# Kernel optimization log

Hardware: AMD Instinct MI355X
Metric: run time of the kernel (lower is better)

Reference implementation:

```python
import jax, jax.numpy as jnp
import numpy as np

N = 50000      # num nodes
E = 800000     # num edges
F_IN = 100     # input features (ogbn-products)
HID = 128      # hidden_dim (per-head out_channels)
H = 2          # heads
OUT = 47       # num classes
NEG_SLOPE = 0.2


def setup_inputs() -> dict:
    key = jax.random.key(0)
    ks = jax.random.split(key, 14)
    def glorot(k, shape, fan):
        return jax.random.normal(k, shape, jnp.float32) * (1.0 / np.sqrt(fan))
    x = jax.random.normal(ks[0], (N, F_IN), jnp.float32)
    edge_index = jax.random.randint(ks[1], (2, E), 0, N)
    # GAT layer 0: lin_l (= lin_r, shared) weight [H*HID, F_IN], attention vecs [H, HID]
    W0 = glorot(ks[2], (H * HID, F_IN), F_IN)
    b0 = jnp.zeros((H * HID,), jnp.float32)
    attl0 = glorot(ks[3], (H, HID), HID)
    attr0 = glorot(ks[4], (H, HID), HID)
    # GAT layer 1: input dim H*HID
    W1 = glorot(ks[5], (H * HID, H * HID), H * HID)
    b1 = jnp.zeros((H * HID,), jnp.float32)
    attl1 = glorot(ks[6], (H, HID), HID)
    attr1 = glorot(ks[7], (H, HID), HID)
    # post_mp: Linear(H*HID -> HID), Linear(HID -> OUT)
    Wp1 = glorot(ks[8], (HID, H * HID), H * HID)
    bp1 = jnp.zeros((HID,), jnp.float32)
    Wp2 = glorot(ks[9], (OUT, HID), HID)
    bp2 = jnp.zeros((OUT,), jnp.float32)
    return dict(x=x, edge_index=edge_index, W0=W0, b0=b0, attl0=attl0, attr0=attr0,
                W1=W1, b1=b1, attl1=attl1, attr1=attr1,
                Wp1=Wp1, bp1=bp1, Wp2=Wp2, bp2=bp2)


def gat_layer(x, W, b, att_l, att_r, src, dst):
    # shared lin_l == lin_r in the source
    h = (x @ W.T + b).reshape(-1, H, HID)          # [N, H, C]
    alpha_l = jnp.einsum('nhc,hc->nh', h, att_l)   # per-node left scores
    alpha_r = jnp.einsum('nhc,hc->nh', h, att_r)   # per-node right scores
    e = jax.nn.leaky_relu(alpha_l[src] + alpha_r[dst], NEG_SLOPE)  # [E, H]
    # segment softmax over edges grouped by destination node
    emax = jax.ops.segment_max(e, dst, num_segments=N)             # [N, H]
    ee = jnp.exp(e - emax[dst])
    denom = jax.ops.segment_sum(ee, dst, num_segments=N)           # [N, H]
    a = ee / denom[dst]                                            # [E, H]
    msg = a[:, :, None] * h[src]                                   # [E, H, C]
    out = jax.ops.segment_sum(msg, dst, num_segments=N)            # [N, H, C]
    return out.reshape(-1, H * HID)


def reference(x, edge_index, W0, b0, attl0, attr0, W1, b1, attl1, attr1, Wp1, bp1, Wp2, bp2):
    src, dst = edge_index[0], edge_index[1]
    x = jax.nn.relu(gat_layer(x, W0, b0, attl0, attr0, src, dst))
    x = jax.nn.relu(gat_layer(x, W1, b1, attl1, attr1, src, dst))
    h = x @ Wp1.T + bp1           # dropout p=0.0 -> identity
    logits = h @ Wp2.T + bp2
    return jax.nn.log_softmax(logits, axis=1)
```

## Files before the change

### kernel.cpp

```cpp
#include <hip/hip_runtime.h>
#include <math.h>

#define N_NODES 50000
#define E_EDGES 800000
#define F_IN 100
#define HID 128
#define HEADS 2
#define OUT_C 47
#define HH (HEADS*HID)
#define MPAD 50048

typedef float floatx4 __attribute__((ext_vector_type(4)));
typedef float float2v __attribute__((ext_vector_type(2)));
typedef short short8 __attribute__((ext_vector_type(8)));

__device__ inline ushort bf16round(float v) {
    unsigned u = __float_as_uint(v);
    return (ushort)((u + 0x7FFFu + ((u >> 16) & 1u)) >> 16);
}

__device__ __forceinline__ void gl_lds16(const void* g, void* l) {
    __builtin_amdgcn_global_load_lds(
        (const __attribute__((address_space(1))) unsigned int*)g,
        (__attribute__((address_space(3))) unsigned int*)l, 16, 0, 0);
}

__device__ __forceinline__ void gemm_body(
    int bx, int by,
    const ushort* __restrict__ Ab, const ushort* __restrict__ Wb,
    const float* __restrict__ bias,
    ushort* __restrict__ Hb,
    const float* __restrict__ attl, const float* __restrict__ attr,
    float* __restrict__ al, float* __restrict__ ar,
    int M, int Kp, ushort* sA, ushort* sB)
{
    const int t = threadIdx.x;
    const int wave = t >> 6, lane = t & 63;
    const int quad = lane >> 4, l16 = lane & 15;
    const int rl = lane >> 2, seg = lane & 3;
    const int m0 = by * 128, n0 = bx * 128;

    floatx4 acc[2][8];
#pragma unroll
    for (int i = 0; i < 2; i++)
#pragma unroll
        for (int j = 0; j < 8; j++) acc[i][j] = (floatx4)(0.f);

    for (int k0 = 0; k0 < Kp; k0 += 32) {
#pragma unroll
        for (int j = 0; j < 2; j++) {
            int br = wave * 32 + j * 16;
            size_t gro = (size_t)(m0 + br + rl) * Kp + k0 + seg * 8;
            gl_lds16(Ab + gro, sA + br * 32);
        }
#pragma unroll
        for (int j = 0; j < 2; j++) {
            int br = wave * 32 + j * 16;
            size_t gro = (size_t)(n0 + br + rl) * Kp + k0 + seg * 8;
            gl_lds16(Wb + gro, sB + br * 32);
        }
        __syncthreads();

        short8 af[2];
#pragma unroll
        for (int sm = 0; sm < 2; sm++) {
            int r = wave * 32 + sm * 16 + l16;
            af[sm] = *(const short8*)(sA + r * 32 + quad * 8);
        }
#pragma unroll
        for (int sn = 0; sn < 8; sn++) {
            int r = sn * 16 + l16;
            short8 b = *(const short8*)(sB + r * 32 + quad * 8);
#pragma unroll
            for (int sm = 0; sm < 2; sm++)
                acc[sm][sn] = __builtin_amdgcn_mfma_f32_16x16x32_bf16(af[sm], b, acc[sm][sn], 0, 0, 0);
        }
        __syncthreads();
    }

    float bias_r[8], att_l[8], att_r[8];
#pragma unroll
    for (int sn = 0; sn < 8; sn++) {
        int ai = n0 + sn * 16 + l16;
        bias_r[sn] = bias[ai];
        att_l[sn] = attl[ai];
        att_r[sn] = attr[ai];
    }
#pragma unroll
    for (int sm = 0; sm < 2; sm++)
#pragma unroll
        for (int r = 0; r < 4; r++) {
            int gm = m0 + wave * 32 + sm * 16 + quad * 4 + r;
            float suml = 0.f, sumr = 0.f;
#pragma unroll
            for (int sn = 0; sn < 8; sn++) {
                float v = acc[sm][sn][r] + bias_r[sn];
                suml += v * att_l[sn];
                sumr += v * att_r[sn];
                if (gm < M) {
                    int gn = n0 + sn * 16 + l16;
                    Hb[(size_t)gm * 256 + gn] = bf16round(v);
                }
            }
#pragma unroll
            for (int off = 1; off < 16; off <<= 1) {
                suml += __shfl_xor(suml, off);
                sumr += __shfl_xor(sumr, off);
            }
            if (l16 == 0 && gm < M) {
                al[gm * HEADS + bx] = suml;
                ar[gm * HEADS + bx] = sumr;
            }
        }
}

__global__ __launch_bounds__(256) void gemm_l0(
    const ushort* __restrict__ xb, const ushort* __restrict__ W0b,
    const float* __restrict__ b0,
    const float* __restrict__ attl0, const float* __restrict__ attr0,
    ushort* __restrict__ hb, float* __restrict__ al, float* __restrict__ ar)
{
    __shared__ ushort sA[128 * 32], sB[128 * 32];
    gemm_body(blockIdx.x, blockIdx.y, xb, W0b, b0,
              hb, attl0, attr0, al, ar, N_NODES, 128, sA, sB);
}

__global__ __launch_bounds__(256) void gemm_l1(
    const ushort* __restrict__ Ab, const ushort* __restrict__ Wb,
    const float* __restrict__ bias, ushort* __restrict__ Hb,
    const float* __restrict__ attl, const float* __restrict__ attr,
    float* __restrict__ al, float* __restrict__ ar)
{
    __shared__ ushort sA[128 * 32], sB[128 * 32];
    gemm_body(blockIdx.x, blockIdx.y, Ab, Wb, bias,
              Hb, attl, attr, al, ar, N_NODES, HH, sA, sB);
}

__global__ void count_convert(const int* __restrict__ dstv, int* __restrict__ deg,
                              ushort* __restrict__ rank,
                              const float* __restrict__ x,  const float* __restrict__ W0,
                              const float* __restrict__ W1, const float* __restrict__ Wp1,
                              const float* __restrict__ Wp2,
                              ushort* __restrict__ xb,  ushort* __restrict__ W0b,
                              ushort* __restrict__ W1b, ushort* __restrict__ Wp1b,
                              ushort* __restrict__ Wp2b) {
    const int cx = N_NODES * 32;
    const int c0 = cx + 256 * 32;
    const int c1 = c0 + (HH * HH) / 4;
    const int c2 = c1 + (HID * HH) / 4;
    const int c3 = c2 + (64 * HID) / 4;
    int i = blockIdx.x * 256 + threadIdx.x;
    if (i < E_EDGES) {
        int d = dstv[i];
        rank[i] = (ushort)atomicAdd(&deg[d], 1);
    }
    if (i >= c3) return;
    float4 v = make_float4(0.f, 0.f, 0.f, 0.f);
    ushort* H; size_t o;
    if (i < cx) {
        int row = i >> 5, kc = (i & 31) * 4;
        if (kc < F_IN) v = *(const float4*)(x + (size_t)row * F_IN + kc);
        H = xb; o = (size_t)row * 128 + kc;
    } else if (i < c0) {
        int j = i - cx;
        int row = j >> 5, kc = (j & 31) * 4;
        if (kc < F_IN) v = *(const float4*)(W0 + (size_t)row * F_IN + kc);
        H = W0b; o = (size_t)row * 128 + kc;
    } else if (i < c1) {
        int j = i - c0;
        v = *(const float4*)(W1 + (size_t)j * 4);
        H = W1b; o = (size_t)j * 4;
    } else if (i < c2) {
        int j = i - c1;
        v = *(const float4*)(Wp1 + (size_t)j * 4);
        H = Wp1b; o = (size_t)j * 4;
    } else {
        int j = i - c2;
        int row = j >> 5;
        if (row < OUT_C) v = *(const float4*)(Wp2 + (size_t)j * 4);
        H = Wp2b; o = (size_t)j * 4;
    }
    ushort4 r;
    r.x = bf16round(v.x); r.y = bf16round(v.y);
    r.z = bf16round(v.z); r.w = bf16round(v.w);
    *(ushort4*)(H + o) = r;
}

__global__ void scan_local(const int* __restrict__ cnt, int* __restrict__ excl,
                           int* __restrict__ bsum, int Nn) {
    __shared__ int s[256];
    int t = threadIdx.x;
    int i = blockIdx.x * 256 + t;
    int v = (i < Nn) ? cnt[i] : 0;
    s[t] = v;
    __syncthreads();
    for (int off = 1; off < 256; off <<= 1) {
        int add = (t >= off) ? s[t - off] : 0;
        __syncthreads();
        s[t] += add;
        __syncthreads();
    }
    int incl = s[t];
    if (i < Nn) excl[i] = incl - v;
    if (t == 255) bsum[blockIdx.x] = incl;
}

__global__ void scan_add_fused(int* __restrict__ rowptr, const int* __restrict__ bsum,
                               int Nn, int Etot, int nblk) {
    __shared__ int s[256];
    int t = threadIdx.x;
    s[t] = (t < nblk) ? bsum[t] : 0;
    __syncthreads();
    for (int off = 1; off < 256; off <<= 1) {
        int add = (t >= off) ? s[t - off] : 0;
        __syncthreads();
        s[t] += add;
        __syncthreads();
    }
    int add = (blockIdx.x == 0) ? 0 : s[blockIdx.x - 1];
    int i = blockIdx.x * 256 + t;
    if (i < Nn) rowptr[i] += add;
    if (i == 0) rowptr[Nn] = Etot;
}

__global__ void fill_csr16(const int* __restrict__ src, const int* __restrict__ dst,
                           const int* __restrict__ rowptr, const ushort* __restrict__ rank,
                           ushort* __restrict__ csr16, int E) {
    int e = blockIdx.x * 256 + threadIdx.x;
    if (e < E) {
        int pos = rowptr[dst[e]] + (int)rank[e];
        csr16[pos] = (ushort)src[e];
    }
}

__global__ __launch_bounds__(256) void gat_aggregate(
    const ushort* __restrict__ hb, const float* __restrict__ al, const float* __restrict__ ar,
    const int* __restrict__ rowptr, const ushort* __restrict__ csr16,
    ushort* __restrict__ outb)
{
    const int node = blockIdx.x * 4 + (threadIdx.x >> 6);
    const int lane = threadIdx.x & 63;
    if (node >= N_NODES) return;
    const int beg = rowptr[node], end = rowptr[node + 1];
    const int half = lane >> 5;
    const int l32  = lane & 31;
    const int headf = l32 >> 4;
    const float2 ard = ((const float2*)ar)[node];

    float dsum0 = 0.f, dsum1 = 0.f;
    float2v av[4];
#pragma unroll
    for (int j = 0; j < 4; j++) av[j] = (float2v)(0.f);

    for (int c0 = beg; c0 < end; c0 += 64) {
        const int n = min(64, end - c0);
        int s = 0; float w0 = 0.f, w1 = 0.f;
        if (lane < n) {
            s = (int)csr16[c0 + lane];
            float2 aa = ((const float2*)al)[s];
            float e0 = aa.x + ard.x;
            float e1 = aa.y + ard.y;
            e0 = fmaxf(e0, 0.f) + 0.2f * fminf(e0, 0.f);
            e1 = fmaxf(e1, 0.f) + 0.2f * fminf(e1, 0.f);
            w0 = __expf(e0); w1 = __expf(e1);
            dsum0 += w0; dsum1 += w1;
        }
        for (int i = 0; i < n; i += 4) {
            int e0i = i + half;
            int   se0 = __shfl(s,  e0i);
            float u00 = __shfl(w0, e0i);
            float u01 = __shfl(w1, e0i);
            float2v we0 = (float2v)(headf ? u01 : u00);
            const uint4 q0 = *(const uint4*)(hb + (size_t)se0 * 256 + l32 * 8);
            int e1i = i + 2 + half;
            int   se1 = __shfl(s,  e1i);
            float u10 = __shfl(w0, e1i);
            float u11 = __shfl(w1, e1i);
            float2v we1 = (float2v)(headf ? u11 : u10);
            const uint4 q1 = *(const uint4*)(hb + (size_t)se1 * 256 + l32 * 8);
            float2v p;
            p.x = __uint_as_float(q0.x << 16); p.y = __uint_as_float(q0.x & 0xFFFF0000u);
            av[0] += we0 * p;
            p.x = __uint_as_float(q0.y << 16); p.y = __uint_as_float(q0.y & 0xFFFF0000u);
            av[1] += we0 * p;
            p.x = __uint_as_float(q0.z << 16); p.y = __uint_as_float(q0.z & 0xFFFF0000u);
            av[2] += we0 * p;
            p.x = __uint_as_float(q0.w << 16); p.y = __uint_as_float(q0.w & 0xFFFF0000u);
            av[3] += we0 * p;
            p.x = __uint_as_float(q1.x << 16); p.y = __uint_as_float(q1.x & 0xFFFF0000u);
            av[0] += we1 * p;
            p.x = __uint_as_float(q1.y << 16); p.y = __uint_as_float(q1.y & 0xFFFF0000u);
            av[1] += we1 * p;
            p.x = __uint_as_float(q1.z << 16); p.y = __uint_as_float(q1.z & 0xFFFF0000u);
            av[2] += we1 * p;
            p.x = __uint_as_float(q1.w << 16); p.y = __uint_as_float(q1.w & 0xFFFF0000u);
            av[3] += we1 * p;
        }
    }
#pragma unroll
    for (int j = 0; j < 4; j++) {
        av[j].x += __shfl_xor(av[j].x, 32);
        av[j].y += __shfl_xor(av[j].y, 32);
    }
#pragma unroll
    for (int off = 32; off; off >>= 1) {
        dsum0 += __shfl_xor(dsum0, off);
        dsum1 += __shfl_xor(dsum1, off);
    }
    if (half == 0) {
        const float den = headf ? dsum1 : dsum0;
        const float inv = (end > beg) ? 1.f / den : 0.f;
        ushort r[8];
#pragma unroll
        for (int j = 0; j < 4; j++) {
            r[2*j]   = bf16round(fmaxf(av[j].x * inv, 0.f));
            r[2*j+1] = bf16round(fmaxf(av[j].y * inv, 0.f));
        }
        *(uint4*)(outb + (size_t)node * 256 + l32 * 8) = *(uint4*)r;
    }
}

__global__ __launch_bounds__(256) void fused_post(
    const ushort* __restrict__ Ab,
    const ushort* __restrict__ Bb,
    const float* __restrict__ bp1,
    const ushort* __restrict__ W2b,
    const float* __restrict__ bp2,
    float* __restrict__ out, int M)
{
    __shared__ ushort sA[128 * 32];
    __shared__ ushort sB[128 * 32];
    __shared__ ushort sP[128 * 136];

    const int t = threadIdx.x;
    const int wave = t >> 6, lane = t & 63;
    const int quad = lane >> 4, l16 = lane & 15;
    const int rl = lane >> 2, seg = lane & 3;
    const int m0 = blockIdx.x * 128;

    floatx4 acc[2][8];
#pragma unroll
    for (int i = 0; i < 2; i++)
#pragma unroll
        for (int j = 0; j < 8; j++) acc[i][j] = (floatx4)(0.f);

    for (int k0 = 0; k0 < HH; k0 += 32) {
#pragma unroll
        for (int j = 0; j < 2; j++) {
            int br = wave * 32 + j * 16;
            size_t gro = (size_t)(m0 + br + rl) * HH + k0 + seg * 8;
            gl_lds16(Ab + gro, sA + br * 32);
        }
#pragma unroll
        for (int j = 0; j < 2; j++) {
            int br = wave * 32 + j * 16;
            size_t gro = (size_t)(br + rl) * HH + k0 + seg * 8;
            gl_lds16(Bb + gro, sB + br * 32);
        }
        __syncthreads();
        short8 af[2];
#pragma unroll
        for (int sm = 0; sm < 2; sm++) {
            int r = wave * 32 + sm * 16 + l16;
            af[sm] = *(const short8*)(sA + r * 32 + quad * 8);
        }
#pragma unroll
        for (int sn = 0; sn < 8; sn++) {
            int r = sn * 16 + l16;
            short8 b = *(const short8*)(sB + r * 32 + quad * 8);
#pragma unroll
            for (int sm = 0; sm < 2; sm++)
                acc[sm][sn] = __builtin_amdgcn_mfma_f32_16x16x32_bf16(af[sm], b, acc[sm][sn], 0, 0, 0);
        }
        __syncthreads();
    }
#pragma unroll
    for (int sm = 0; sm < 2; sm++)
#pragma unroll
        for (int sn = 0; sn < 8; sn++)
#pragma unroll
            for (int r = 0; r < 4; r++) {
                int row = wave * 32 + sm * 16 + quad * 4 + r;
                int col = sn * 16 + l16;
                sP[row * 136 + col] = bf16round(acc[sm][sn][r] + bp1[col]);
            }
    __syncthreads();

    floatx4 acc2[2][4];
#pragma unroll
    for (int i = 0; i < 2; i++)
#pragma unroll
        for (int j = 0; j < 4; j++) acc2[i][j] = (floatx4)(0.f);

    for (int k0 = 0; k0 < HID; k0 += 32) {
        {
            int br = wave * 16;
            size_t gro = (size_t)(br + rl) * HID + k0 + seg * 8;
            gl_lds16(W2b + gro, sA + br * 32);
        }
        __syncthreads();
        short8 ph[2];
#pragma unroll
        for (int sm = 0; sm < 2; sm++) {
            int r = wave * 32 + sm * 16 + l16;
            ph[sm] = *(const short8*)(sP + r * 136 + k0 + quad * 8);
        }
#pragma unroll
        for (int sn = 0; sn < 4; sn++) {
            int r = sn * 16 + l16;
            short8 b = *(const short8*)(sA + r * 32 + quad * 8);
#pragma unroll
            for (int sm = 0; sm < 2; sm++)
                acc2[sm][sn] = __builtin_amdgcn_mfma_f32_16x16x32_bf16(ph[sm], b, acc2[sm][sn], 0, 0, 0);
        }
        __syncthreads();
    }

    float b2[4];
#pragma unroll
    for (int sn = 0; sn < 4; sn++) {
        int n = sn * 16 + l16;
        b2[sn] = (n < OUT_C) ? bp2[n] : 0.f;
    }
#pragma unroll
    for (int sm = 0; sm < 2; sm++)
#pragma unroll
        for (int r = 0; r < 4; r++) {
            float v[4];
            float m = -INFINITY;
#pragma unroll
            for (int sn = 0; sn < 4; sn++) {
                int n = sn * 16 + l16;
                float xv = (n < OUT_C) ? acc2[sm][sn][r] + b2[sn] : -INFINITY;
                v[sn] = xv;
                m = fmaxf(m, xv);
            }
#pragma unroll
            for (int off = 1; off < 16; off <<= 1) m = fmaxf(m, __shfl_xor(m, off));
            float ssum = 0.f;
#pragma unroll
            for (int sn = 0; sn < 4; sn++) {
                int n = sn * 16 + l16;
                if (n < OUT_C) ssum += __expf(v[sn] - m);
            }
#pragma unroll
            for (int off = 1; off < 16; off <<= 1) ssum += __shfl_xor(ssum, off);
            float lse = m + logf(ssum);
            int gm = m0 + wave * 32 + sm * 16 + quad * 4 + r;
            if (gm < M) {
#pragma unroll
                for (int sn = 0; sn < 4; sn++) {
                    int n = sn * 16 + l16;
                    if (n < OUT_C) out[(size_t)gm * OUT_C + n] = v[sn] - lse;
                }
            }
        }
}

extern "C" void kernel_launch(void* const* d_in, const int* in_sizes, int n_in,
                              void* d_out, int out_size, void* d_ws, size_t ws_size,
                              hipStream_t stream) {
    const float* x     = (const float*)d_in[0];
    const int*   ei    = (const int*)d_in[1];
    const float* W0    = (const float*)d_in[2];
    const float* b0    = (const float*)d_in[3];
    const float* attl0 = (const float*)d_in[4];
    const float* attr0 = (const float*)d_in[5];
    const float* W1    = (const float*)d_in[6];
    const float* b1    = (const float*)d_in[7];
    const float* attl1 = (const float*)d_in[8];
    const float* attr1 = (const float*)d_in[9];
    const float* Wp1   = (const float*)d_in[10];
    const float* bp1   = (const float*)d_in[11];
    const float* Wp2   = (const float*)d_in[12];
    const float* bp2   = (const float*)d_in[13];
    float* out = (float*)d_out;

    const int Nn = N_NODES, Etot = E_EDGES;
    const int* srcv = ei;
    const int* dstv = ei + Etot;

    char* ws = (char*)d_ws;
    size_t off = 0;
    auto alloc = [&](size_t bytes) -> void* {
        void* p = ws + off;
        off = (off + bytes + 255) & ~(size_t)255;
        return p;
    };
    int*    rowptr = (int*)alloc((size_t)(Nn + 1) * sizeof(int));
    int*    deg    = (int*)alloc((size_t)Nn * sizeof(int));
    ushort* rank   = (ushort*)alloc((size_t)Etot * 2);
    ushort* csr16  = (ushort*)alloc((size_t)Etot * 2);
    int*    bsum   = (int*)alloc(256 * sizeof(int));
    float*  al     = (float*)alloc((size_t)Nn * HEADS * sizeof(float));
    float*  ar     = (float*)alloc((size_t)Nn * HEADS * sizeof(float));
    ushort* xb     = (ushort*)alloc((size_t)MPAD * 128 * 2);
    ushort* W0b    = (ushort*)alloc((size_t)HH * 128 * 2);
    ushort* W1b    = (ushort*)alloc((size_t)HH * HH * 2);
    ushort* Wp1b   = (ushort*)alloc((size_t)HID * HH * 2);
    ushort* Wp2b   = (ushort*)alloc((size_t)64 * HID * 2);
    ushort* hb     = (ushort*)alloc((size_t)Nn * HH * 2);
    ushort* xbb    = (ushort*)alloc((size_t)MPAD * HH * 2);

    const int nblk = (Nn + 255) / 256;

    hipMemsetAsync(deg, 0, (size_t)Nn * sizeof(int), stream);

    {
        const int tot = N_NODES * 32 + 256 * 32 + (HH * HH) / 4 + (HID * HH) / 4 + (64 * HID) / 4;
        const int grid = (tot + 255) / 256;
        count_convert<<<grid, 256, 0, stream>>>(
            dstv, deg, rank, x, W0, W1, Wp1, Wp2, xb, W0b, W1b, Wp1b, Wp2b);
    }

    {
        dim3 g(2, MPAD / 128);
        gemm_l0<<<g, 256, 0, stream>>>(xb, W0b, b0, attl0, attr0, hb, al, ar);
    }

    scan_local<<<nblk, 256, 0, stream>>>(deg, rowptr, bsum, Nn);
    scan_add_fused<<<nblk, 256, 0, stream>>>(rowptr, bsum, Nn, Etot, nblk);
    fill_csr16<<<(Etot + 255) / 256, 256, 0, stream>>>(srcv, dstv, rowptr, rank, csr16, Etot);

    gat_aggregate<<<(Nn + 3) / 4, 256, 0, stream>>>(hb, al, ar, rowptr, csr16, xbb);

    {
        dim3 g(2, MPAD / 128);
        gemm_l1<<<g, 256, 0, stream>>>(xbb, W1b, b1, hb, attl1, attr1, al, ar);
    }
    gat_aggregate<<<(Nn + 3) / 4, 256, 0, stream>>>(hb, al, ar, rowptr, csr16, xbb);

    fused_post<<<MPAD / 128, 256, 0, stream>>>(xbb, Wp1b, bp1, Wp2b, bp2, out, Nn);
}
```

Measured before the change: 316.5 us.

## Split GAT aggregation into one wave per head, one block per node

The aggregation kernel now gives each head its own 64-lane wave and each node its own 128-thread block, where before one wave handled both heads of a node. Each wave gathers 256-byte half-rows, so 4 edges are in flight per instruction instead of 2. Per-head scoring and the reduction are simplified. The cost is that every edge's source index and attention score are loaded twice, once per head, the grid has many more small blocks, and partial chunks need masked loads.

```diff
diff --git a/kernel.cpp b/kernel.cpp
--- a/kernel.cpp
+++ b/kernel.cpp
@@ -233,51 +233,46 @@
     }
 }
 
-__global__ __launch_bounds__(256) void gat_aggregate(
+__global__ __launch_bounds__(128) void gat_aggregate(
     const ushort* __restrict__ hb, const float* __restrict__ al, const float* __restrict__ ar,
     const int* __restrict__ rowptr, const ushort* __restrict__ csr16,
     ushort* __restrict__ outb)
 {
-    const int node = blockIdx.x * 4 + (threadIdx.x >> 6);
+    const int node = blockIdx.x;
+    const int head = threadIdx.x >> 6;
     const int lane = threadIdx.x & 63;
-    if (node >= N_NODES) return;
+    const int q = lane >> 4, c = lane & 15;
     const int beg = rowptr[node], end = rowptr[node + 1];
-    const int half = lane >> 5;
-    const int l32  = lane & 31;
-    const int headf = l32 >> 4;
-    const float2 ard = ((const float2*)ar)[node];
-
-    float dsum0 = 0.f, dsum1 = 0.f;
+    const float ard = ar[node * HEADS + head];
+    const ushort* __restrict__ hbh = hb + head * HID + c * 8;
+
+    float dsum = 0.f;
     float2v av[4];
 #pragma unroll
     for (int j = 0; j < 4; j++) av[j] = (float2v)(0.f);
 
     for (int c0 = beg; c0 < end; c0 += 64) {
         const int n = min(64, end - c0);
-        int s = 0; float w0 = 0.f, w1 = 0.f;
+        int s = 0; float w = 0.f;
         if (lane < n) {
             s = (int)csr16[c0 + lane];
-            float2 aa = ((const float2*)al)[s];
-            float e0 = aa.x + ard.x;
-            float e1 = aa.y + ard.y;
-            e0 = fmaxf(e0, 0.f) + 0.2f * fminf(e0, 0.f);
-            e1 = fmaxf(e1, 0.f) + 0.2f * fminf(e1, 0.f);
-            w0 = __expf(e0); w1 = __expf(e1);
-            dsum0 += w0; dsum1 += w1;
-        }
-        for (int i = 0; i < n; i += 4) {
-            int e0i = i + half;
-            int   se0 = __shfl(s,  e0i);
-            float u00 = __shfl(w0, e0i);
-            float u01 = __shfl(w1, e0i);
-            float2v we0 = (float2v)(headf ? u01 : u00);
-            const uint4 q0 = *(const uint4*)(hb + (size_t)se0 * 256 + l32 * 8);
-            int e1i = i + 2 + half;
-            int   se1 = __shfl(s,  e1i);
-            float u10 = __shfl(w0, e1i);
-            float u11 = __shfl(w1, e1i);
-            float2v we1 = (float2v)(headf ? u11 : u10);
-            const uint4 q1 = *(const uint4*)(hb + (size_t)se1 * 256 + l32 * 8);
+            float e = al[s * HEADS + head] + ard;
+            e = fmaxf(e, 0.f) + 0.2f * fminf(e, 0.f);
+            w = __expf(e);
+            dsum += w;
+        }
+        for (int i = 0; i < n; i += 8) {
+            int e0 = i + q, e1 = i + 4 + q;
+            int   s0 = __shfl(s, e0);
+            float w0 = __shfl(w, e0);
+            int   s1 = __shfl(s, e1);
+            float w1 = __shfl(w, e1);
+            uint4 q0 = make_uint4(0u, 0u, 0u, 0u);
+            uint4 q1 = make_uint4(0u, 0u, 0u, 0u);
+            if (e0 < n) q0 = *(const uint4*)(hbh + (size_t)s0 * 256);
+            if (e1 < n) q1 = *(const uint4*)(hbh + (size_t)s1 * 256);
+            float2v we0 = (float2v)(w0);
+            float2v we1 = (float2v)(w1);
             float2v p;
             p.x = __uint_as_float(q0.x << 16); p.y = __uint_as_float(q0.x & 0xFFFF0000u);
             av[0] += we0 * p;
@@ -299,24 +294,23 @@
     }
 #pragma unroll
     for (int j = 0; j < 4; j++) {
+        av[j].x += __shfl_xor(av[j].x, 16);
+        av[j].y += __shfl_xor(av[j].y, 16);
         av[j].x += __shfl_xor(av[j].x, 32);
         av[j].y += __shfl_xor(av[j].y, 32);
     }
 #pragma unroll
-    for (int off = 32; off; off >>= 1) {
-        dsum0 += __shfl_xor(dsum0, off);
-        dsum1 += __shfl_xor(dsum1, off);
-    }
-    if (half == 0) {
-        const float den = headf ? dsum1 : dsum0;
-        const float inv = (end > beg) ? 1.f / den : 0.f;
+    for (int off = 32; off; off >>= 1) dsum += __shfl_xor(dsum, off);
+
+    if (q == 0) {
+        const float inv = (end > beg) ? 1.f / dsum : 0.f;
         ushort r[8];
 #pragma unroll
         for (int j = 0; j < 4; j++) {
             r[2*j]   = bf16round(fmaxf(av[j].x * inv, 0.f));
             r[2*j+1] = bf16round(fmaxf(av[j].y * inv, 0.f));
         }
-        *(uint4*)(outb + (size_t)node * 256 + l32 * 8) = *(uint4*)r;
+        *(uint4*)(outb + (size_t)node * 256 + head * HID + c * 8) = *(uint4*)r;
     }
 }
 
@@ -522,13 +516,13 @@
     scan_add_fused<<<nblk, 256, 0, stream>>>(rowptr, bsum, Nn, Etot, nblk);
     fill_csr16<<<(Etot + 255) / 256, 256, 0, stream>>>(srcv, dstv, rowptr, rank, csr16, Etot);
 
-    gat_aggregate<<<(Nn + 3) / 4, 256, 0, stream>>>(hb, al, ar, rowptr, csr16, xbb);
+    gat_aggregate<<<Nn, 128, 0, stream>>>(hb, al, ar, rowptr, csr16, xbb);
 
     {
         dim3 g(2, MPAD / 128);
         gemm_l1<<<g, 256, 0, stream>>>(xbb, W1b, b1, hb, attl1, attr1, al, ar);
     }
-    gat_aggregate<<<(Nn + 3) / 4, 256, 0, stream>>>(hb, al, ar, rowptr, csr16, xbb);
+    gat_aggregate<<<Nn, 128, 0, stream>>>(hb, al, ar, rowptr, csr16, xbb);
 
     fused_post<<<MPAD / 128, 256, 0, stream>>>(xbb, Wp1b, bp1, Wp2b, bp2, out, Nn);
 }
```

Result: no change. 313.4 us (-1.0%).
